# Kernel optimization log

Hardware: AMD Instinct MI355X
Metric: run time of the kernel (lower is better)

Reference implementation:

```python
import jax, jax.numpy as jnp
import numpy as np

B, N, HID = 2, 2048, 1024
H, DH = 16, 64

def apply_rope(x, rope):
    # x: [B,H,N,D], rope: [B,N,D] interpreted as interleaved (cos, sin) pairs
    Bx, Hx, Nx, D = x.shape
    xp = x.reshape(Bx, Hx, Nx, D // 2, 2)
    rp = rope.reshape(Bx, 1, Nx, D // 2, 2)
    cos, sin = rp[..., 0], rp[..., 1]
    x0, x1 = xp[..., 0], xp[..., 1]
    out = jnp.stack([x0 * cos - x1 * sin, x1 * cos + x0 * sin], axis=-1)
    return out.reshape(Bx, Hx, Nx, D)


def setup_inputs() -> dict:
    key = jax.random.key(0)
    k1, k2, k3, k4 = jax.random.split(key, 4)
    x = jax.random.normal(k1, (B, N, HID), dtype=jnp.float32)
    rope = jax.random.normal(k2, (B, N, DH), dtype=jnp.float32)
    Wqkv = jax.random.normal(k3, (3 * H * DH, HID), dtype=jnp.float32) * (HID ** -0.5)
    Wout = jax.random.normal(k4, (HID, H * DH), dtype=jnp.float32) * ((H * DH) ** -0.5)
    return {"x": x, "rope": rope, "Wqkv": Wqkv, "Wout": Wout}


def reference(x, rope, Wqkv, Wout):
    scale = DH ** -0.5
    qkv = jnp.einsum('bnd,ed->bne', x, Wqkv)          # [B,N,3*H*DH]
    qkv = qkv.reshape(B, N, 3, H, DH)
    qkv = jnp.transpose(qkv, (2, 0, 3, 1, 4))          # [3,B,H,N,DH]
    q, k, v = qkv[0], qkv[1], qkv[2]
    q = apply_rope(q, rope)
    k = apply_rope(k, rope)
    attn = jnp.einsum('bhnd,bhmd->bhnm', q, k) * scale  # [B,H,N,N]
    attn = jax.nn.softmax(attn, axis=-1)
    out = jnp.einsum('bhnm,bhmd->bhnd', attn, v)        # [B,H,N,DH]
    out = jnp.transpose(out, (0, 2, 1, 3)).reshape(B, N, H * DH)
    return jnp.einsum('bne,de->bnd', out, Wout)
```

## Files before the change

### kernel.cpp

```cpp
#include <hip/hip_runtime.h>
#include <stdint.h>
#include <stddef.h>

typedef __bf16 bf16;
typedef __bf16 bf16x2 __attribute__((ext_vector_type(2)));
typedef __bf16 bf16x4 __attribute__((ext_vector_type(4)));
typedef __bf16 bf16x8 __attribute__((ext_vector_type(8)));
typedef float f32x2 __attribute__((ext_vector_type(2)));
typedef float f32x4 __attribute__((ext_vector_type(4)));
typedef float f32x16 __attribute__((ext_vector_type(16)));

constexpr int Bb = 2, Nn = 2048, HID = 1024, Hh = 16, DH = 64;
constexpr int MTOK = Bb * Nn;
constexpr int E3 = 3 * Hh * DH;

__global__ void cast_kernel(const float* __restrict__ in, bf16* __restrict__ out, int n4) {
  int i = blockIdx.x * blockDim.x + threadIdx.x;
  if (i >= n4) return;
  f32x4 v = reinterpret_cast<const f32x4*>(in)[i];
  bf16x4 o;
#pragma unroll
  for (int j = 0; j < 4; ++j) o[j] = (bf16)v[j];
  reinterpret_cast<bf16x4*>(out)[i] = o;
}

template <bool OUT_BF16>
__global__ __launch_bounds__(256) void gemm_bt(const bf16* __restrict__ A,
                                               const bf16* __restrict__ Bt,
                                               void* __restrict__ Cp,
                                               int M, int N, int K) {
  __shared__ __align__(16) bf16 As[128 * 32];
  __shared__ __align__(16) bf16 Bs[128 * 32];
  const int tid = threadIdx.x;
  const int lane = tid & 63;
  const int wave = tid >> 6;
  const int wr = wave >> 1, wc = wave & 1;
  const int bm = blockIdx.x, bn = blockIdx.y;
  const int frow = lane & 15;
  const int fk = (lane >> 4) * 8;
  const int c0 = wave * 128 + lane;

  f32x4 acc[4][4] = {};

  for (int k0 = 0; k0 < K; k0 += 32) {
#pragma unroll
    for (int i = 0; i < 2; ++i) {
      int c = c0 + i * 64;
      int row = c >> 2;
      int col = (c & 3) * 8;
      const bf16* ga = A + (size_t)(bm * 128 + row) * K + k0 + col;
      const bf16* gb = Bt + (size_t)(bn * 128 + row) * K + k0 + col;
      __builtin_amdgcn_global_load_lds((const __attribute__((address_space(1))) void*)ga,
                                       (__attribute__((address_space(3))) void*)(As + c * 8),
                                       16, 0, 0);
      __builtin_amdgcn_global_load_lds((const __attribute__((address_space(1))) void*)gb,
                                       (__attribute__((address_space(3))) void*)(Bs + c * 8),
                                       16, 0, 0);
    }
    __syncthreads();
    bf16x8 af[4], bfr[4];
#pragma unroll
    for (int m = 0; m < 4; ++m)
      af[m] = *reinterpret_cast<const bf16x8*>(As + (wr * 64 + m * 16 + frow) * 32 + fk);
#pragma unroll
    for (int n = 0; n < 4; ++n)
      bfr[n] = *reinterpret_cast<const bf16x8*>(Bs + (wc * 64 + n * 16 + frow) * 32 + fk);
#pragma unroll
    for (int m = 0; m < 4; ++m)
#pragma unroll
      for (int n = 0; n < 4; ++n)
        acc[m][n] = __builtin_amdgcn_mfma_f32_16x16x32_bf16(af[m], bfr[n], acc[m][n], 0, 0, 0);
    __syncthreads();
  }

  const int r0 = bm * 128 + wr * 64;
  const int cc0 = bn * 128 + wc * 64;
#pragma unroll
  for (int m = 0; m < 4; ++m)
#pragma unroll
    for (int n = 0; n < 4; ++n)
#pragma unroll
      for (int r = 0; r < 4; ++r) {
        int row = r0 + m * 16 + (lane >> 4) * 4 + r;
        int col = cc0 + n * 16 + frow;
        if (OUT_BF16)
          ((bf16*)Cp)[(size_t)row * N + col] = (bf16)acc[m][n][r];
        else
          ((float*)Cp)[(size_t)row * N + col] = acc[m][n][r];
      }
}

__global__ __launch_bounds__(256) void rope_pack(const bf16* __restrict__ qkvb,
                                                 const float* __restrict__ rope,
                                                 bf16* __restrict__ qpk,
                                                 bf16* __restrict__ kpk,
                                                 bf16* __restrict__ vpk) {
  __shared__ bf16 qs[128][66];
  __shared__ bf16 ks[128][66];
  __shared__ bf16 vs[128][66];
  const int bh = blockIdx.y;
  const int b = bh >> 4;
  const int h = bh & 15;
  const int n0 = blockIdx.x * 128;
  const int t = threadIdx.x;

  for (int it = 0; it < 16; ++it) {
    int p = it * 256 + t;
    int nl = p >> 5, i = p & 31;
    int n = n0 + nl;
    size_t rowbase = (size_t)(b * Nn + n);
    const bf16* src = qkvb + rowbase * E3 + h * DH + 2 * i;
    f32x2 cs = *reinterpret_cast<const f32x2*>(rope + rowbase * DH + 2 * i);
    float c = cs[0], sn = cs[1];
    bf16x2 qv = *reinterpret_cast<const bf16x2*>(src);
    bf16x2 kv = *reinterpret_cast<const bf16x2*>(src + HID);
    bf16x2 vv = *reinterpret_cast<const bf16x2*>(src + 2 * HID);
    float q0 = (float)qv[0], q1 = (float)qv[1];
    float k0 = (float)kv[0], k1 = (float)kv[1];
    qs[nl][2 * i]     = (bf16)(q0 * c - q1 * sn);
    qs[nl][2 * i + 1] = (bf16)(q1 * c + q0 * sn);
    ks[nl][2 * i]     = (bf16)(k0 * c - k1 * sn);
    ks[nl][2 * i + 1] = (bf16)(k1 * c + k0 * sn);
    vs[nl][2 * i]     = vv[0];
    vs[nl][2 * i + 1] = vv[1];
  }
  __syncthreads();

  const int lane2 = t & 63;
  const int dd = t >> 6;
  const int lo2 = lane2 & 31, hi2 = lane2 >> 5;
#pragma unroll
  for (int kbq = 0; kbq < 4; ++kbq) {
    int row = kbq * 32 + lo2;
    int col = dd * 16 + hi2 * 8;
    bf16x8 q8 = *reinterpret_cast<const bf16x8*>(&qs[row][col]);
    bf16x8 k8 = *reinterpret_cast<const bf16x8*>(&ks[row][col]);
    size_t base = ((((size_t)bh * 64 + (n0 >> 5) + kbq) * 4 + dd) * 64 + lane2) * 8;
    *reinterpret_cast<bf16x8*>(qpk + base) = q8;
    *reinterpret_cast<bf16x8*>(kpk + base) = k8;
  }

#pragma unroll
  for (int wi = 0; wi < 4; ++wi) {
    int id = wi * 256 + t;
    int lane3 = id & 63;
    int sub = id >> 6;
    int kt = sub >> 3, dt = (sub >> 2) & 1, kbi = sub & 3;
    int lo3 = lane3 & 31, hi3 = lane3 >> 5;
    bf16x8 v8;
#pragma unroll
    for (int j = 0; j < 8; ++j)
      v8[j] = vs[kt * 64 + kbi * 16 + hi3 * 8 + j][dt * 32 + lo3];
    size_t vbase = ((((size_t)bh * 32 + (n0 >> 6) + kt) * 8 + dt * 4 + kbi) * 64 + lane3) * 8;
    *reinterpret_cast<bf16x8*>(vpk + vbase) = v8;
  }
}

__global__ __launch_bounds__(256, 2) void attn_kernel(const bf16* __restrict__ qpk,
                                                      const bf16* __restrict__ kpk,
                                                      const bf16* __restrict__ vpk,
                                                      bf16* __restrict__ outb) {
  const int lane = threadIdx.x & 63;
  const int wave = threadIdx.x >> 6;
  const int bid = blockIdx.x;
  const int xcd = bid & 7;
  const int idx = bid >> 3;
  const int bh = xcd * 4 + (idx >> 4);
  const int qt = idx & 15;
  const int b = bh >> 4, h = bh & 15;
  const int lo = lane & 31;
  const int hi = lane >> 5;
  const int q0 = qt * 128 + wave * 32;

  constexpr float SCL = 0.125f * 1.44269504088896340736f;

  bf16x8 qf[4];
#pragma unroll
  for (int d = 0; d < 4; ++d)
    qf[d] = *reinterpret_cast<const bf16x8*>(
        qpk + ((((size_t)bh * 64 + qt * 4 + wave) * 4 + d) * 64 + lane) * 8);

  f32x16 o0 = {}, o1 = {};
  float mrun = -3e38f, lrun = 0.f;

  auto cvtpk = [](float a, float b) {
    unsigned w;
    asm("v_cvt_pk_bf16_f32 %0, %1, %2" : "=v"(w) : "v"(a), "v"(b));
    return w;
  };

  auto loadK64 = [&](int key0, bf16x8* kf) {
    size_t base = (((size_t)bh * 64 + (key0 >> 5)) * 4 * 64 + lane) * 8;
#pragma unroll
    for (int half = 0; half < 2; ++half)
#pragma unroll
      for (int d = 0; d < 4; ++d)
        kf[half * 4 + d] = *reinterpret_cast<const bf16x8*>(
            kpk + base + (half * 4 + d) * 512);
  };

  auto tilestep64 = [&](int key0, const bf16x8* kf) {
    bf16x8 vf[8];
    size_t vbase = (((size_t)bh * 32 + (key0 >> 6)) * 8 * 64 + lane) * 8;
#pragma unroll
    for (int sub = 0; sub < 8; ++sub)
      vf[sub] = *reinterpret_cast<const bf16x8*>(vpk + vbase + sub * 512);

    f32x16 s0 = {}, s1 = {};
#pragma unroll
    for (int d = 0; d < 4; ++d) {
      s0 = __builtin_amdgcn_mfma_f32_32x32x16_bf16(kf[d], qf[d], s0, 0, 0, 0);
      s1 = __builtin_amdgcn_mfma_f32_32x32x16_bf16(kf[4 + d], qf[d], s1, 0, 0, 0);
    }

    float t16[16];
#pragma unroll
    for (int r = 0; r < 16; ++r) t16[r] = fmaxf(s0[r], s1[r]);
#pragma unroll
    for (int r = 0; r < 8; ++r) t16[r] = fmaxf(t16[r], t16[r + 8]);
#pragma unroll
    for (int r = 0; r < 4; ++r) t16[r] = fmaxf(t16[r], t16[r + 4]);
    float tmv = fmaxf(fmaxf(t16[0], t16[2]), fmaxf(t16[1], t16[3]));
    float tm = fmaxf(tmv, __shfl_xor(tmv, 32));
    float tms = tm * SCL;

    if (__any(tms > mrun + 8.0f)) {
      float mn = fmaxf(mrun, tms);
      float corr = __builtin_amdgcn_exp2f(mrun - mn);
      mrun = mn;
      lrun *= corr;
#pragma unroll
      for (int r = 0; r < 16; ++r) { o0[r] *= corr; o1[r] *= corr; }
    }

    float e[32];
#pragma unroll
    for (int r = 0; r < 16; ++r) e[r] = __builtin_amdgcn_exp2f(fmaf(s0[r], SCL, -mrun));
#pragma unroll
    for (int r = 0; r < 16; ++r) e[16 + r] = __builtin_amdgcn_exp2f(fmaf(s1[r], SCL, -mrun));

    float u[16];
#pragma unroll
    for (int r = 0; r < 16; ++r) u[r] = e[r] + e[16 + r];
#pragma unroll
    for (int r = 0; r < 8; ++r) u[r] += u[r + 8];
#pragma unroll
    for (int r = 0; r < 4; ++r) u[r] += u[r + 4];
    float tsv = (u[0] + u[2]) + (u[1] + u[3]);
    lrun += tsv + __shfl_xor(tsv, 32);

    union { unsigned w[4]; bf16x8 v8; } pb[4];
#pragma unroll
    for (int kbi = 0; kbi < 4; ++kbi) {
      const int eo = (kbi >> 1) * 16 + (kbi & 1) * 8;
      unsigned X0 = cvtpk(e[eo + 0], e[eo + 1]);
      unsigned X1 = cvtpk(e[eo + 2], e[eo + 3]);
      unsigned Y0 = cvtpk(e[eo + 4], e[eo + 5]);
      unsigned Y1 = cvtpk(e[eo + 6], e[eo + 7]);
      unsigned S0 = hi ? X0 : Y0;
      unsigned S1 = hi ? X1 : Y1;
      unsigned T0 = __shfl_xor(S0, 32);
      unsigned T1 = __shfl_xor(S1, 32);
      pb[kbi].w[0] = hi ? T0 : X0;
      pb[kbi].w[1] = hi ? T1 : X1;
      pb[kbi].w[2] = hi ? Y0 : T0;
      pb[kbi].w[3] = hi ? Y1 : T1;
    }

#pragma unroll
    for (int kbi = 0; kbi < 4; ++kbi) {
      o0 = __builtin_amdgcn_mfma_f32_32x32x16_bf16(vf[kbi], pb[kbi].v8, o0, 0, 0, 0);
      o1 = __builtin_amdgcn_mfma_f32_32x32x16_bf16(vf[4 + kbi], pb[kbi].v8, o1, 0, 0, 0);
    }
  };

  bf16x8 kA[8], kB[8];
  loadK64(0, kA);
  for (int t = 0; t < 32; t += 2) {
    loadK64((t + 1) * 64, kB);
    __builtin_amdgcn_sched_barrier(0);
    tilestep64(t * 64, kA);
    int n2 = (t + 2 < 32) ? (t + 2) * 64 : 0;
    loadK64(n2, kA);
    __builtin_amdgcn_sched_barrier(0);
    tilestep64((t + 1) * 64, kB);
  }

  float invl = 1.0f / lrun;
#pragma unroll
  for (int dt = 0; dt < 2; ++dt) {
#pragma unroll
    for (int g = 0; g < 4; ++g) {
      bf16x4 ov;
#pragma unroll
      for (int j = 0; j < 4; ++j) {
        float val = (dt ? o1[g * 4 + j] : o0[g * 4 + j]) * invl;
        ov[j] = (bf16)val;
      }
      int dh = dt * 32 + g * 8 + hi * 4;
      *reinterpret_cast<bf16x4*>(outb + (size_t)(b * Nn + q0 + lo) * HID + h * DH + dh) = ov;
    }
  }
}

extern "C" void kernel_launch(void* const* d_in, const int* in_sizes, int n_in,
                              void* d_out, int out_size, void* d_ws, size_t ws_size,
                              hipStream_t stream) {
  const float* x = (const float*)d_in[0];
  const float* rope = (const float*)d_in[1];
  const float* Wqkv = (const float*)d_in[2];
  const float* Wout = (const float*)d_in[3];
  float* out = (float*)d_out;

  char* w = (char*)d_ws;
  size_t off = 0;
  auto alloc = [&](size_t bytes) -> void* {
    void* p = w + off;
    off += (bytes + 255) & ~(size_t)255;
    return p;
  };
  bf16* xb    = (bf16*)alloc((size_t)MTOK * HID * 2);
  bf16* wqkvb = (bf16*)alloc((size_t)E3 * HID * 2);
  bf16* woutb = (bf16*)alloc((size_t)HID * HID * 2);
  bf16* qkvb  = (bf16*)alloc((size_t)MTOK * E3 * 2);
  bf16* qpk   = (bf16*)alloc((size_t)Bb * Hh * Nn * DH * 2);
  bf16* kpk   = (bf16*)alloc((size_t)Bb * Hh * Nn * DH * 2);
  bf16* vpk   = (bf16*)alloc((size_t)Bb * Hh * Nn * DH * 2);
  bf16* attno = (bf16*)alloc((size_t)MTOK * HID * 2);

  cast_kernel<<<(MTOK * HID / 4) / 256, 256, 0, stream>>>(x, xb, MTOK * HID / 4);
  cast_kernel<<<(E3 * HID / 4) / 256, 256, 0, stream>>>(Wqkv, wqkvb, E3 * HID / 4);
  cast_kernel<<<(HID * HID / 4) / 256, 256, 0, stream>>>(Wout, woutb, HID * HID / 4);

  gemm_bt<true><<<dim3(MTOK / 128, E3 / 128), 256, 0, stream>>>(xb, wqkvb, qkvb, MTOK, E3, HID);

  rope_pack<<<dim3(Nn / 128, Bb * Hh), 256, 0, stream>>>(qkvb, rope, qpk, kpk, vpk);

  attn_kernel<<<dim3(512), 256, 0, stream>>>(qpk, kpk, vpk, attno);

  gemm_bt<false><<<dim3(MTOK / 128, HID / 128), 256, 0, stream>>>(attno, woutb, out, MTOK, HID, HID);
}
```

Measured before the change: 143.8 us.

## Split attention KV range in two and add a combine kernel

The attention kernel now splits each query tile's key range into two halves, so the grid doubles to 1024 blocks. Each block writes unnormalized fp32 partial outputs plus its running max and sum to a workspace. A new combine kernel merges the two halves with log-sum-exp rescaling and writes the bf16 output. Launch bounds rise to 4 blocks per SM. The goal is more parallelism and occupancy on the 256-CU device, paid for with extra global traffic for the fp32 partials, an extra kernel launch, and possible register pressure.

```diff
diff --git a/kernel.cpp b/kernel.cpp
--- a/kernel.cpp
+++ b/kernel.cpp
@@ -13,6 +13,7 @@
 constexpr int Bb = 2, Nn = 2048, HID = 1024, Hh = 16, DH = 64;
 constexpr int MTOK = Bb * Nn;
 constexpr int E3 = 3 * Hh * DH;
+constexpr int NROW = 32 * Nn;
 
 __global__ void cast_kernel(const float* __restrict__ in, bf16* __restrict__ out, int n4) {
   int i = blockIdx.x * blockDim.x + threadIdx.x;
@@ -156,21 +157,23 @@
   }
 }
 
-__global__ __launch_bounds__(256, 2) void attn_kernel(const bf16* __restrict__ qpk,
+__global__ __launch_bounds__(256, 4) void attn_kernel(const bf16* __restrict__ qpk,
                                                       const bf16* __restrict__ kpk,
                                                       const bf16* __restrict__ vpk,
-                                                      bf16* __restrict__ outb) {
+                                                      float* __restrict__ opart,
+                                                      float* __restrict__ mlbuf) {
   const int lane = threadIdx.x & 63;
   const int wave = threadIdx.x >> 6;
   const int bid = blockIdx.x;
   const int xcd = bid & 7;
   const int idx = bid >> 3;
-  const int bh = xcd * 4 + (idx >> 4);
-  const int qt = idx & 15;
-  const int b = bh >> 4, h = bh & 15;
+  const int bh = xcd * 4 + (idx >> 5);
+  const int qt = (idx >> 1) & 15;
+  const int split = idx & 1;
   const int lo = lane & 31;
   const int hi = lane >> 5;
   const int q0 = qt * 128 + wave * 32;
+  const int kbase = split * 1024;
 
   constexpr float SCL = 0.125f * 1.44269504088896340736f;
 
@@ -275,32 +278,57 @@
   };
 
   bf16x8 kA[8], kB[8];
-  loadK64(0, kA);
-  for (int t = 0; t < 32; t += 2) {
-    loadK64((t + 1) * 64, kB);
+  loadK64(kbase, kA);
+  for (int t = 0; t < 16; t += 2) {
+    loadK64(kbase + (t + 1) * 64, kB);
     __builtin_amdgcn_sched_barrier(0);
-    tilestep64(t * 64, kA);
-    int n2 = (t + 2 < 32) ? (t + 2) * 64 : 0;
+    tilestep64(kbase + t * 64, kA);
+    int n2 = (t + 2 < 16) ? kbase + (t + 2) * 64 : kbase;
     loadK64(n2, kA);
     __builtin_amdgcn_sched_barrier(0);
-    tilestep64((t + 1) * 64, kB);
-  }
-
-  float invl = 1.0f / lrun;
+    tilestep64(kbase + (t + 1) * 64, kB);
+  }
+
+  const size_t row = (size_t)bh * Nn + q0 + lo;
+  float* op = opart + ((size_t)split * NROW + row) * 64;
 #pragma unroll
   for (int dt = 0; dt < 2; ++dt) {
 #pragma unroll
     for (int g = 0; g < 4; ++g) {
-      bf16x4 ov;
-#pragma unroll
-      for (int j = 0; j < 4; ++j) {
-        float val = (dt ? o1[g * 4 + j] : o0[g * 4 + j]) * invl;
-        ov[j] = (bf16)val;
-      }
-      int dh = dt * 32 + g * 8 + hi * 4;
-      *reinterpret_cast<bf16x4*>(outb + (size_t)(b * Nn + q0 + lo) * HID + h * DH + dh) = ov;
-    }
-  }
+      f32x4 ov;
+#pragma unroll
+      for (int j = 0; j < 4; ++j) ov[j] = dt ? o1[g * 4 + j] : o0[g * 4 + j];
+      *reinterpret_cast<f32x4*>(op + dt * 32 + g * 8 + hi * 4) = ov;
+    }
+  }
+  if (hi == 0) {
+    f32x2 mlv;
+    mlv[0] = mrun;
+    mlv[1] = lrun;
+    *reinterpret_cast<f32x2*>(mlbuf + ((size_t)split * NROW + row) * 2) = mlv;
+  }
+}
+
+__global__ __launch_bounds__(256) void attn_combine(const float* __restrict__ opart,
+                                                    const float* __restrict__ mlbuf,
+                                                    bf16* __restrict__ attno) {
+  int gid = blockIdx.x * 256 + threadIdx.x;
+  int row = gid >> 4;
+  int dc = (gid & 15) << 2;
+  int bh = row >> 11, q = row & 2047;
+  int b = bh >> 4, h = bh & 15;
+  f32x2 v0 = *reinterpret_cast<const f32x2*>(mlbuf + (size_t)row * 2);
+  f32x2 v1 = *reinterpret_cast<const f32x2*>(mlbuf + ((size_t)NROW + row) * 2);
+  float ms = fmaxf(v0[0], v1[0]);
+  float c0 = __builtin_amdgcn_exp2f(v0[0] - ms);
+  float c1 = __builtin_amdgcn_exp2f(v1[0] - ms);
+  f32x4 a = *reinterpret_cast<const f32x4*>(opart + (size_t)row * 64 + dc);
+  f32x4 bb = *reinterpret_cast<const f32x4*>(opart + ((size_t)NROW + row) * 64 + dc);
+  float inv = 1.0f / (v0[1] * c0 + v1[1] * c1);
+  bf16x4 o;
+#pragma unroll
+  for (int j = 0; j < 4; ++j) o[j] = (bf16)((a[j] * c0 + bb[j] * c1) * inv);
+  *reinterpret_cast<bf16x4*>(attno + ((size_t)(b * Nn + q)) * HID + h * DH + dc) = o;
 }
 
 extern "C" void kernel_launch(void* const* d_in, const int* in_sizes, int n_in,
@@ -327,6 +355,8 @@
   bf16* kpk   = (bf16*)alloc((size_t)Bb * Hh * Nn * DH * 2);
   bf16* vpk   = (bf16*)alloc((size_t)Bb * Hh * Nn * DH * 2);
   bf16* attno = (bf16*)alloc((size_t)MTOK * HID * 2);
+  float* opart = (float*)alloc((size_t)2 * NROW * 64 * 4);
+  float* mlbuf = (float*)alloc((size_t)2 * NROW * 2 * 4);
 
   cast_kernel<<<(MTOK * HID / 4) / 256, 256, 0, stream>>>(x, xb, MTOK * HID / 4);
   cast_kernel<<<(E3 * HID / 4) / 256, 256, 0, stream>>>(Wqkv, wqkvb, E3 * HID / 4);
@@ -336,7 +366,9 @@
 
   rope_pack<<<dim3(Nn / 128, Bb * Hh), 256, 0, stream>>>(qkvb, rope, qpk, kpk, vpk);
 
-  attn_kernel<<<dim3(512), 256, 0, stream>>>(qpk, kpk, vpk, attno);
+  attn_kernel<<<dim3(1024), 256, 0, stream>>>(qpk, kpk, vpk, opart, mlbuf);
+
+  attn_combine<<<dim3(NROW * 16 / 256), 256, 0, stream>>>(opart, mlbuf, attno);
 
   gemm_bt<false><<<dim3(MTOK / 128, HID / 128), 256, 0, stream>>>(attno, woutb, out, MTOK, HID, HID);
 }
```

After: 280.8 us. 1.95x slower.
